# Optimization experiments

Measured on AMD Instinct MI355X. Metric: run time of the kernel, lower is better.

## Reference

```python
import jax, jax.numpy as jnp
import numpy as np

# --- module hyperparameters (from RealMNISTModel.setup) ---
HIDDEN = 1024          # hidden_dim (init kwarg)
NUM_CLASSES = 10
H_HARM = 32            # PhasorBankJAX H
DELTA0 = 7.0           # PhasorBankJAX delta0
DECAY = 0.7            # SpikingAttentionJAX decay
THETA = 1.0            # SpikingAttentionJAX theta
K_WINNERS = 5          # SpikingAttentionJAX k_winners
K_TOP = 32             # K = min(32, hidden_dim)


def setup_inputs() -> dict:
    key = jax.random.key(0)
    ks = jax.random.split(key, 4)
    B, D = 16384, 28 * 28
    x = jax.random.normal(ks[0], (B, 28, 28), jnp.float32)
    W_in = jax.random.normal(ks[1], (D, HIDDEN), jnp.float32) / np.float32(np.sqrt(D))
    b_in = jnp.zeros((HIDDEN,), jnp.float32)
    W_ph = jax.random.normal(ks[2], (2 * H_HARM, HIDDEN), jnp.float32) / np.float32(np.sqrt(2 * H_HARM))
    b_ph = jnp.zeros((HIDDEN,), jnp.float32)
    W_out = jax.random.normal(ks[3], (HIDDEN, NUM_CLASSES), jnp.float32) / np.float32(np.sqrt(HIDDEN))
    b_out = jnp.zeros((NUM_CLASSES,), jnp.float32)
    return {"x": x, "W_in": W_in, "b_in": b_in, "W_ph": W_ph, "b_ph": b_ph,
            "W_out": W_out, "b_out": b_out}


def _phasor_bank(s):
    # PhasorBankJAX: scalar phase input -> H harmonics of cos/sin -> [2H]
    phases = s * DELTA0 * jnp.arange(1, H_HARM + 1, dtype=jnp.float32)
    return jnp.concatenate([jnp.cos(phases), jnp.sin(phases)])


def _spiking_gains(tokens, vocab_size):
    # SpikingAttentionJAX: LIF membrane over vocab driven by token spikes,
    # k-winners-take-all gain vector. tokens: [K] int32.
    def step(V, t):
        V = V * DECAY
        V = V.at[t].add(1.0)
        spiked = V >= THETA
        V = jnp.where(spiked, V - THETA, V)  # reset-by-subtraction
        return V, None
    V, _ = jax.lax.scan(step, jnp.zeros((vocab_size,), jnp.float32), tokens)
    _, win_idx = jax.lax.top_k(V, K_WINNERS)
    return 1.0 + jnp.zeros((vocab_size,), jnp.float32).at[win_idx].set(1.0)


def reference(x, W_in, b_in, W_ph, b_ph, W_out, b_out):
    B = x.shape[0]
    x_flat = x.reshape((B, -1))                      # [B, 784]
    projected = x_flat @ W_in + b_in                 # [B, HIDDEN]
    x_mean = jnp.mean(projected, axis=-1)            # [B]
    temporal = jax.vmap(_phasor_bank)(x_mean)        # [B, 2H]
    enhanced = projected + (temporal @ W_ph + b_ph)  # [B, HIDDEN]
    vocab_size = enhanced.shape[-1]
    topk_idx = jax.lax.top_k(enhanced, K_TOP)[1].astype(jnp.int32)  # [B, K]
    gains = jax.vmap(_spiking_gains, in_axes=(0, None))(topk_idx, vocab_size)
    attended = enhanced * gains
    return attended @ W_out + b_out                  # [B, NUM_CLASSES]
```

## Files before the change

kernel.cpp:

```cpp
#include <hip/hip_runtime.h>
#include <math.h>

#define DHID   784
#define HID    1024
#define NB     10
#define MC_LD  800
#define M2_OFF (11*MC_LD)
#define M2_LD  12
#define C0_OFF (M2_OFF + 64*M2_LD)
#define WS_FLOATS 9600
#define DELTA0 7.0f

__global__ void prep_kernel(const float* __restrict__ W_in,
                            const float* __restrict__ b_in,
                            const float* __restrict__ W_ph,
                            const float* __restrict__ b_ph,
                            const float* __restrict__ W_out,
                            const float* __restrict__ b_out,
                            float* __restrict__ ws) {
  const int b = blockIdx.x;
  const int l = threadIdx.x;

  float acc[11];
#pragma unroll
  for (int c = 0; c < 11; ++c) acc[c] = 0.f;

  for (int j = l; j < HID; j += 64) {
    float w, extra;
    if (b < DHID)            { w = W_in[b*HID + j];          extra = w;       }
    else if (b < DHID + 64)  { w = W_ph[(b - DHID)*HID + j]; extra = 0.f;     }
    else                     { w = b_in[j] + b_ph[j];        extra = b_in[j]; }
    const float wg = (j < 5) ? 2.0f * w : w;
    const float2* wrow = (const float2*)(W_out + (size_t)j * NB);
#pragma unroll
    for (int p = 0; p < 5; ++p) {
      float2 w2 = wrow[p];
      acc[2*p]     += wg * w2.x;
      acc[2*p + 1] += wg * w2.y;
    }
    acc[10] += extra;
  }

#pragma unroll
  for (int c = 0; c < 11; ++c) {
    float v = acc[c];
    v += __shfl_xor(v, 1,  64);
    v += __shfl_xor(v, 2,  64);
    v += __shfl_xor(v, 4,  64);
    v += __shfl_xor(v, 8,  64);
    v += __shfl_xor(v, 16, 64);
    v += __shfl_xor(v, 32, 64);
    acc[c] = v;
  }

  if (l == 0) {
    if (b < DHID) {
#pragma unroll
      for (int c = 0; c < 10; ++c) ws[c*MC_LD + b] = acc[c];
      ws[10*MC_LD + b] = acc[10] * (1.0f / HID);
    } else if (b < DHID + 64) {
      const int h = b - DHID;
#pragma unroll
      for (int c = 0; c < 10; ++c) ws[M2_OFF + h*M2_LD + c] = acc[c];
      ws[M2_OFF + h*M2_LD + 10] = 0.f;
      ws[M2_OFF + h*M2_LD + 11] = 0.f;
    } else {
#pragma unroll
      for (int c = 0; c < 10; ++c) ws[C0_OFF + c] = acc[c] + b_out[c];
      ws[C0_OFF + 10] = acc[10] * (1.0f / HID);
    }
  }
}

__device__ __forceinline__ void row_tail(int row, const float* a,
                                         const float* lds, float* out,
                                         int kl, float bmean) {
  const float m    = a[10] + bmean;
  const float base = DELTA0 * m;
  float s1, c1, s2, c2;
  __sincosf((float)(kl + 1)  * base, &s1, &c1);
  __sincosf((float)(kl + 17) * base, &s2, &c2);
  const float* m2a = &lds[M2_OFF + (kl)      * M2_LD];
  const float* m2b = &lds[M2_OFF + (kl + 16) * M2_LD];
  const float* m2c = &lds[M2_OFF + (kl + 32) * M2_LD];
  const float* m2d = &lds[M2_OFF + (kl + 48) * M2_LD];
  float t[10];
#pragma unroll
  for (int c = 0; c < 10; ++c)
    t[c] = c1 * m2a[c] + c2 * m2b[c] + s1 * m2c[c] + s2 * m2d[c];
#pragma unroll
  for (int c = 0; c < 10; ++c) {
    float v = t[c];
    v += __shfl_xor(v, 1, 64);
    v += __shfl_xor(v, 2, 64);
    v += __shfl_xor(v, 4, 64);
    v += __shfl_xor(v, 8, 64);
    t[c] = v;
  }
  if (kl == 0) {
#pragma unroll
    for (int c = 0; c < 10; ++c)
      out[row * NB + c] = a[c] + t[c] + lds[C0_OFF + c];
  }
}

__global__ __launch_bounds__(256) void main_kernel(const float* __restrict__ x,
                                                   const float* __restrict__ ws,
                                                   float* __restrict__ out) {
  __shared__ float lds[WS_FLOATS];
  const int tid = threadIdx.x;

  for (int idx = tid; idx < WS_FLOATS / 4; idx += 256)
    ((float4*)lds)[idx] = ((const float4*)ws)[idx];
  __syncthreads();

  const int wav  = tid >> 6;
  const int lane = tid & 63;
  const int kl   = lane & 15;
  const int rsub = lane >> 4;
  const int row  = blockIdx.x * 32 + wav * 8 + rsub * 2;
  const float* x0 = x + (size_t)row * DHID;

  float a0[11], a1[11];
#pragma unroll
  for (int c = 0; c < 11; ++c) { a0[c] = 0.f; a1[c] = 0.f; }

#pragma unroll
  for (int i = 0; i < 13; ++i) {
    const int d = 4 * kl + 64 * i;
    if (d < DHID) {
      const float4 xa = *(const float4*)(x0 + d);
      const float4 xb = *(const float4*)(x0 + DHID + d);
#pragma unroll
      for (int c = 0; c < 11; ++c) {
        const float4 mv = *(const float4*)(&lds[c * MC_LD + d]);
        a0[c] += xa.x * mv.x + xa.y * mv.y + xa.z * mv.z + xa.w * mv.w;
        a1[c] += xb.x * mv.x + xb.y * mv.y + xb.z * mv.z + xb.w * mv.w;
      }
    }
  }

#pragma unroll
  for (int c = 0; c < 11; ++c) {
    float v = a0[c];
    v += __shfl_xor(v, 1, 64);
    v += __shfl_xor(v, 2, 64);
    v += __shfl_xor(v, 4, 64);
    v += __shfl_xor(v, 8, 64);
    a0[c] = v;
    float u = a1[c];
    u += __shfl_xor(u, 1, 64);
    u += __shfl_xor(u, 2, 64);
    u += __shfl_xor(u, 4, 64);
    u += __shfl_xor(u, 8, 64);
    a1[c] = u;
  }

  const float bmean = lds[C0_OFF + 10];
  row_tail(row,     a0, lds, out, kl, bmean);
  row_tail(row + 1, a1, lds, out, kl, bmean);
}

extern "C" void kernel_launch(void* const* d_in, const int* in_sizes, int n_in,
                              void* d_out, int out_size, void* d_ws, size_t ws_size,
                              hipStream_t stream) {
  const float* x     = (const float*)d_in[0];
  const float* W_in  = (const float*)d_in[1];
  const float* b_in  = (const float*)d_in[2];
  const float* W_ph  = (const float*)d_in[3];
  const float* b_ph  = (const float*)d_in[4];
  const float* W_out = (const float*)d_in[5];
  const float* b_out = (const float*)d_in[6];
  float* out = (float*)d_out;
  float* ws  = (float*)d_ws;

  prep_kernel<<<DHID + 64 + 1, 64, 0, stream>>>(W_in, b_in, W_ph, b_ph,
                                                W_out, b_out, ws);
  main_kernel<<<512, 256, 0, stream>>>(x, ws, out);
}
```

Before: 40.68 us.

## Stage W_out in LDS for prep and process four rows per lane group

The prep kernel now packs four weight rows per 256-thread block and stages W_out into shared memory with a padded stride, instead of re-reading it from global memory in every 64-thread block. The main kernel has each 16-lane group handle four rows instead of two, so every LDS fragment of the folded weights is reused across more rows, and it launches half as many blocks. The M2 stride is padded to 13 to avoid LDS bank conflicts. The trade-off is higher register pressure, which may lower occupancy, and fewer blocks in flight on a GPU with many compute units.

Result: faster. 39.85 us (-2.0%).

```diff
diff --git a/kernel.cpp b/kernel.cpp
--- a/kernel.cpp
+++ b/kernel.cpp
@@ -6,38 +6,46 @@
 #define NB     10
 #define MC_LD  800
 #define M2_OFF (11*MC_LD)
-#define M2_LD  12
+#define M2_LD  13
 #define C0_OFF (M2_OFF + 64*M2_LD)
-#define WS_FLOATS 9600
+#define WS_FLOATS 9648
 #define DELTA0 7.0f
 
-__global__ void prep_kernel(const float* __restrict__ W_in,
-                            const float* __restrict__ b_in,
-                            const float* __restrict__ W_ph,
-                            const float* __restrict__ b_ph,
-                            const float* __restrict__ W_out,
-                            const float* __restrict__ b_out,
-                            float* __restrict__ ws) {
-  const int b = blockIdx.x;
-  const int l = threadIdx.x;
+__global__ __launch_bounds__(256) void prep_kernel(
+    const float* __restrict__ W_in,  const float* __restrict__ b_in,
+    const float* __restrict__ W_ph,  const float* __restrict__ b_ph,
+    const float* __restrict__ W_out, const float* __restrict__ b_out,
+    float* __restrict__ ws) {
+  __shared__ float wlds[HID * 11];
+  const int tid = threadIdx.x;
+
+  for (int idx = tid; idx < HID * NB; idx += 256) {
+    const int j = idx / NB;
+    const int c = idx - j * NB;
+    wlds[j * 11 + c] = W_out[idx];
+  }
+  __syncthreads();
+
+  const int w = tid >> 6;
+  const int l = tid & 63;
+  const int b = blockIdx.x * 4 + w;
+  if (b > DHID + 64) return;
 
   float acc[11];
 #pragma unroll
   for (int c = 0; c < 11; ++c) acc[c] = 0.f;
 
-  for (int j = l; j < HID; j += 64) {
-    float w, extra;
-    if (b < DHID)            { w = W_in[b*HID + j];          extra = w;       }
-    else if (b < DHID + 64)  { w = W_ph[(b - DHID)*HID + j]; extra = 0.f;     }
-    else                     { w = b_in[j] + b_ph[j];        extra = b_in[j]; }
-    const float wg = (j < 5) ? 2.0f * w : w;
-    const float2* wrow = (const float2*)(W_out + (size_t)j * NB);
-#pragma unroll
-    for (int p = 0; p < 5; ++p) {
-      float2 w2 = wrow[p];
-      acc[2*p]     += wg * w2.x;
-      acc[2*p + 1] += wg * w2.y;
-    }
+#pragma unroll 4
+  for (int it = 0; it < 16; ++it) {
+    const int j = l + 64 * it;
+    float wv, extra;
+    if (b < DHID)           { wv = W_in[b * HID + j];          extra = wv;      }
+    else if (b < DHID + 64) { wv = W_ph[(b - DHID) * HID + j]; extra = 0.f;     }
+    else                    { wv = b_in[j] + b_ph[j];          extra = b_in[j]; }
+    const float wg = (j < 5) ? 2.0f * wv : wv;
+    const float* wr = &wlds[j * 11];
+#pragma unroll
+    for (int c = 0; c < 10; ++c) acc[c] += wg * wr[c];
     acc[10] += extra;
   }
 
@@ -56,14 +64,15 @@
   if (l == 0) {
     if (b < DHID) {
 #pragma unroll
-      for (int c = 0; c < 10; ++c) ws[c*MC_LD + b] = acc[c];
-      ws[10*MC_LD + b] = acc[10] * (1.0f / HID);
+      for (int c = 0; c < 10; ++c) ws[c * MC_LD + b] = acc[c];
+      ws[10 * MC_LD + b] = acc[10] * (1.0f / HID);
     } else if (b < DHID + 64) {
       const int h = b - DHID;
 #pragma unroll
-      for (int c = 0; c < 10; ++c) ws[M2_OFF + h*M2_LD + c] = acc[c];
-      ws[M2_OFF + h*M2_LD + 10] = 0.f;
-      ws[M2_OFF + h*M2_LD + 11] = 0.f;
+      for (int c = 0; c < 10; ++c) ws[M2_OFF + h * M2_LD + c] = acc[c];
+      ws[M2_OFF + h * M2_LD + 10] = 0.f;
+      ws[M2_OFF + h * M2_LD + 11] = 0.f;
+      ws[M2_OFF + h * M2_LD + 12] = 0.f;
     } else {
 #pragma unroll
       for (int c = 0; c < 10; ++c) ws[C0_OFF + c] = acc[c] + b_out[c];
@@ -118,47 +127,63 @@
   const int lane = tid & 63;
   const int kl   = lane & 15;
   const int rsub = lane >> 4;
-  const int row  = blockIdx.x * 32 + wav * 8 + rsub * 2;
+  const int row  = blockIdx.x * 64 + wav * 16 + rsub * 4;
   const float* x0 = x + (size_t)row * DHID;
 
-  float a0[11], a1[11];
-#pragma unroll
-  for (int c = 0; c < 11; ++c) { a0[c] = 0.f; a1[c] = 0.f; }
-
-#pragma unroll
-  for (int i = 0; i < 13; ++i) {
+  float a0[11], a1[11], a2[11], a3[11];
+#pragma unroll
+  for (int c = 0; c < 11; ++c) { a0[c] = 0.f; a1[c] = 0.f; a2[c] = 0.f; a3[c] = 0.f; }
+
+#pragma unroll 6
+  for (int i = 0; i < 12; ++i) {
     const int d = 4 * kl + 64 * i;
-    if (d < DHID) {
-      const float4 xa = *(const float4*)(x0 + d);
-      const float4 xb = *(const float4*)(x0 + DHID + d);
-#pragma unroll
-      for (int c = 0; c < 11; ++c) {
-        const float4 mv = *(const float4*)(&lds[c * MC_LD + d]);
-        a0[c] += xa.x * mv.x + xa.y * mv.y + xa.z * mv.z + xa.w * mv.w;
-        a1[c] += xb.x * mv.x + xb.y * mv.y + xb.z * mv.z + xb.w * mv.w;
-      }
+    const float4 xa = *(const float4*)(x0 + d);
+    const float4 xb = *(const float4*)(x0 + DHID + d);
+    const float4 xc = *(const float4*)(x0 + 2 * DHID + d);
+    const float4 xd = *(const float4*)(x0 + 3 * DHID + d);
+#pragma unroll
+    for (int c = 0; c < 11; ++c) {
+      const float4 mv = *(const float4*)(&lds[c * MC_LD + d]);
+      a0[c] += xa.x * mv.x + xa.y * mv.y + xa.z * mv.z + xa.w * mv.w;
+      a1[c] += xb.x * mv.x + xb.y * mv.y + xb.z * mv.z + xb.w * mv.w;
+      a2[c] += xc.x * mv.x + xc.y * mv.y + xc.z * mv.z + xc.w * mv.w;
+      a3[c] += xd.x * mv.x + xd.y * mv.y + xd.z * mv.z + xd.w * mv.w;
     }
   }
+  if (kl < 4) {
+    const int d = 768 + 4 * kl;
+    const float4 xa = *(const float4*)(x0 + d);
+    const float4 xb = *(const float4*)(x0 + DHID + d);
+    const float4 xc = *(const float4*)(x0 + 2 * DHID + d);
+    const float4 xd = *(const float4*)(x0 + 3 * DHID + d);
+#pragma unroll
+    for (int c = 0; c < 11; ++c) {
+      const float4 mv = *(const float4*)(&lds[c * MC_LD + d]);
+      a0[c] += xa.x * mv.x + xa.y * mv.y + xa.z * mv.z + xa.w * mv.w;
+      a1[c] += xb.x * mv.x + xb.y * mv.y + xb.z * mv.z + xb.w * mv.w;
+      a2[c] += xc.x * mv.x + xc.y * mv.y + xc.z * mv.z + xc.w * mv.w;
+      a3[c] += xd.x * mv.x + xd.y * mv.y + xd.z * mv.z + xd.w * mv.w;
+    }
+  }
 
 #pragma unroll
   for (int c = 0; c < 11; ++c) {
-    float v = a0[c];
-    v += __shfl_xor(v, 1, 64);
-    v += __shfl_xor(v, 2, 64);
-    v += __shfl_xor(v, 4, 64);
-    v += __shfl_xor(v, 8, 64);
-    a0[c] = v;
-    float u = a1[c];
-    u += __shfl_xor(u, 1, 64);
-    u += __shfl_xor(u, 2, 64);
-    u += __shfl_xor(u, 4, 64);
-    u += __shfl_xor(u, 8, 64);
-    a1[c] = u;
+    float v;
+    v = a0[c]; v += __shfl_xor(v,1,64); v += __shfl_xor(v,2,64);
+    v += __shfl_xor(v,4,64); v += __shfl_xor(v,8,64); a0[c] = v;
+    v = a1[c]; v += __shfl_xor(v,1,64); v += __shfl_xor(v,2,64);
+    v += __shfl_xor(v,4,64); v += __shfl_xor(v,8,64); a1[c] = v;
+    v = a2[c]; v += __shfl_xor(v,1,64); v += __shfl_xor(v,2,64);
+    v += __shfl_xor(v,4,64); v += __shfl_xor(v,8,64); a2[c] = v;
+    v = a3[c]; v += __shfl_xor(v,1,64); v += __shfl_xor(v,2,64);
+    v += __shfl_xor(v,4,64); v += __shfl_xor(v,8,64); a3[c] = v;
   }
 
   const float bmean = lds[C0_OFF + 10];
   row_tail(row,     a0, lds, out, kl, bmean);
   row_tail(row + 1, a1, lds, out, kl, bmean);
+  row_tail(row + 2, a2, lds, out, kl, bmean);
+  row_tail(row + 3, a3, lds, out, kl, bmean);
 }
 
 extern "C" void kernel_launch(void* const* d_in, const int* in_sizes, int n_in,
@@ -174,7 +199,7 @@
   float* out = (float*)d_out;
   float* ws  = (float*)d_ws;
 
-  prep_kernel<<<DHID + 64 + 1, 64, 0, stream>>>(W_in, b_in, W_ph, b_ph,
-                                                W_out, b_out, ws);
-  main_kernel<<<512, 256, 0, stream>>>(x, ws, out);
-}
+  prep_kernel<<<(DHID + 64 + 1 + 3) / 4, 256, 0, stream>>>(W_in, b_in, W_ph, b_ph,
+                                                           W_out, b_out, ws);
+  main_kernel<<<256, 256, 0, stream>>>(x, ws, out);
+}
```
